# Optimization experiments

Measured on AMD Instinct MI355X. Metric: run time of the kernel, lower is better.

## Reference

```python
import jax, jax.numpy as jnp
import numpy as np

T, B, DIM, LATENT, OUT = 512, 1024, 128, 256, 64


def setup_inputs() -> dict:
    key = jax.random.key(0)
    ks = jax.random.split(key, 6)
    s_i = 1.0 / np.sqrt(DIM)
    s_h = 1.0 / np.sqrt(LATENT)
    return {
        "x": jax.random.normal(ks[0], (T, B, DIM), dtype=jnp.float32),
        "h": jnp.zeros((B, LATENT), dtype=jnp.float32),
        "Wi": jax.random.uniform(ks[1], (DIM, LATENT), jnp.float32, -s_i, s_i),
        "bi": jax.random.uniform(ks[2], (LATENT,), jnp.float32, -s_i, s_i),
        "Wh": jax.random.uniform(ks[3], (LATENT, LATENT), jnp.float32, -s_h, s_h),
        "Wd": jax.random.uniform(ks[4], (LATENT, OUT), jnp.float32, -s_h, s_h),
        "bd": jax.random.uniform(ks[5], (OUT,), jnp.float32, -s_h, s_h),
    }


def reference(x, h, Wi, bi, Wh, Wd, bd):
    # Precompute input projections for all steps in one big GEMM: [T,B,latent]
    xi = jnp.einsum("tbd,dl->tbl", x, Wi) + bi

    def step(h, xi_t):
        h = jnp.tanh(xi_t + h @ Wh)
        return h, None

    h_final, _ = jax.lax.scan(step, h, xi)
    return jax.nn.sigmoid(h_final @ Wd + bd)
```

## Files before the change

### kernel.cpp

```cpp
#include <hip/hip_runtime.h>
#include <cmath>
#include <cstdint>

constexpr int T_STEPS = 512;
constexpr int BATCH   = 1024;
constexpr int DIM     = 128;
constexpr int LATENT  = 256;
constexpr int OUT_DIM = 64;
constexpr int ROWS    = 16;
constexpr int NKSUB   = 48;

typedef __attribute__((ext_vector_type(8))) short bf16x8;
typedef __attribute__((ext_vector_type(4))) float f32x4;

__device__ __forceinline__ uint32_t f2bf(float f) {
    uint32_t u = __builtin_bit_cast(uint32_t, f);
    return (u + 0x7FFFu + ((u >> 16) & 1u)) >> 16;
}
__device__ __forceinline__ float bf2f(uint32_t b) {
    return __builtin_bit_cast(float, b << 16);
}
__device__ __forceinline__ uint32_t pk2(float a, float b) {
    return f2bf(a) | (f2bf(b) << 16);
}
__device__ __forceinline__ float fast_tanh(float v) {
    float e = __builtin_amdgcn_exp2f(v * 2.885390081777927f);
    return __builtin_fmaf(-2.0f, __builtin_amdgcn_rcpf(e + 1.0f), 1.0f);
}
__device__ __forceinline__ float fast_sigmoid(float v) {
    float e = __builtin_amdgcn_exp2f(v * -1.4426950408889634f);
    return __builtin_amdgcn_rcpf(e + 1.0f);
}

__global__ __launch_bounds__(512)
void rnn_mfma_w8t2(const float* __restrict__ x,
                   const float* __restrict__ h0,
                   const float* __restrict__ Wi,
                   const float* __restrict__ bi,
                   const float* __restrict__ Wh,
                   const float* __restrict__ Wd,
                   const float* __restrict__ bd,
                   float* __restrict__ out)
{
    __shared__ uint16_t als[2][NKSUB * 128];

    const int tid   = threadIdx.x;
    const int lane  = tid & 63;
    const int wv    = tid >> 6;
    const int b0    = blockIdx.x * ROWS;
    const int row16 = lane & 15;
    const int kgrp  = lane >> 4;
    const int col0  = (wv << 5) + row16;

#define LOADB(NAME, P)                                                      \
    bf16x8 NAME; {                                                          \
        const float* _p = (P);                                              \
        NAME[0] = (short)f2bf(_p[0]);                                       \
        NAME[1] = (short)f2bf(_p[1 * LATENT]);                              \
        NAME[2] = (short)f2bf(_p[2 * LATENT]);                              \
        NAME[3] = (short)f2bf(_p[3 * LATENT]);                              \
        NAME[4] = (short)f2bf(_p[4 * LATENT]);                              \
        NAME[5] = (short)f2bf(_p[5 * LATENT]);                              \
        NAME[6] = (short)f2bf(_p[6 * LATENT]);                              \
        NAME[7] = (short)f2bf(_p[7 * LATENT]);                              \
    }
#define BPH(KK, CT) (Wh + (size_t)((KK) * 32 + kgrp * 8) * LATENT + col0 + ((CT) << 4))
#define BPX(KK, CT) (Wi + (size_t)(((KK) - 8) * 32 + kgrp * 8) * LATENT + col0 + ((CT) << 4))
#define DECL2H(KK) LOADB(B##KK##_0, BPH(KK,0)) LOADB(B##KK##_1, BPH(KK,1))
#define DECL2X(KK) LOADB(B##KK##_0, BPX(KK,0)) LOADB(B##KK##_1, BPX(KK,1))
    DECL2H(0) DECL2H(1) DECL2H(2)  DECL2H(3)
    DECL2H(4) DECL2H(5) DECL2H(6)  DECL2H(7)
    DECL2X(8) DECL2X(9) DECL2X(10) DECL2X(11)

    const float cb0 = bi[col0];
    const float cb1 = bi[col0 + 16];

    const int pr = tid & 15;
    const int pq = tid >> 4;
    {
        const float* hrow = h0 + (size_t)(b0 + pr) * LATENT + (pq << 3);
        float4 a0 = reinterpret_cast<const float4*>(hrow)[0];
        float4 a1 = reinterpret_cast<const float4*>(hrow)[1];
        *reinterpret_cast<uint4*>(&als[0][(pq * 16 + pr) * 8]) =
            make_uint4(pk2(a0.x, a0.y), pk2(a0.z, a0.w),
                       pk2(a1.x, a1.y), pk2(a1.z, a1.w));
        const float* xrow = x + (size_t)(b0 + pr) * DIM + (pq << 2);
        float4 xv = *reinterpret_cast<const float4*>(xrow);
        uint2* dx = reinterpret_cast<uint2*>(
            &als[0][((32 + (pq >> 1)) * 16 + pr) * 8 + ((pq & 1) << 2)]);
        *dx = make_uint2(pk2(xv.x, xv.y), pk2(xv.z, xv.w));
    }
    __syncthreads();

    const int aoff = kgrp * 128 + row16 * 8;
    const float* xp = x + ((size_t)BATCH + b0 + pr) * DIM + (pq << 2);
    const int xwb = ((32 + (pq >> 1)) * 16 + pr) * 8 + ((pq & 1) << 2);

    int cur = 0;
    for (int t = 0; t < T_STEPS; ++t) {
        const bool pf = (t + 1 < T_STEPS);
        float4 xv;
        if (pf) {
            xv = *reinterpret_cast<const float4*>(xp);
            xp += (size_t)BATCH * DIM;
        }

        f32x4 c0 = {cb0, cb0, cb0, cb0};
        f32x4 c1 = {cb1, cb1, cb1, cb1};
        const uint16_t* ab = &als[cur][aoff];
#define MSTEP(KK) {                                                         \
        const bf16x8 a = *reinterpret_cast<const bf16x8*>(ab + (KK) * 512); \
        c0 = __builtin_amdgcn_mfma_f32_16x16x32_bf16(a, B##KK##_0, c0, 0, 0, 0); \
        c1 = __builtin_amdgcn_mfma_f32_16x16x32_bf16(a, B##KK##_1, c1, 0, 0, 0); }
        MSTEP(0) MSTEP(1) MSTEP(2)  MSTEP(3)
        MSTEP(4) MSTEP(5) MSTEP(6)  MSTEP(7)
        MSTEP(8) MSTEP(9) MSTEP(10) MSTEP(11)

        const int nxt = cur ^ 1;
#define WB(CT, CV) {                                                        \
        const int col = col0 + ((CT) << 4);                                 \
        uint16_t* hw = &als[nxt][(col >> 3) * 128 + (col & 7)];             \
        hw[(kgrp * 4 + 0) * 8] = (uint16_t)f2bf(fast_tanh(CV[0]));          \
        hw[(kgrp * 4 + 1) * 8] = (uint16_t)f2bf(fast_tanh(CV[1]));          \
        hw[(kgrp * 4 + 2) * 8] = (uint16_t)f2bf(fast_tanh(CV[2]));          \
        hw[(kgrp * 4 + 3) * 8] = (uint16_t)f2bf(fast_tanh(CV[3])); }
        WB(0, c0) WB(1, c1)

        if (pf)
            *reinterpret_cast<uint2*>(&als[nxt][xwb]) =
                make_uint2(pk2(xv.x, xv.y), pk2(xv.z, xv.w));

        __syncthreads();
        cur = nxt;
    }

    {
        const int o  = tid & 63;
        const int rb = tid >> 6;
        float s0 = bd[o], s1 = s0;
        const uint16_t* hb = als[cur];
        #pragma unroll 8
        for (int k = 0; k < LATENT; k += 2) {
            const float w0 = Wd[(size_t)k * OUT_DIM + o];
            const float w1 = Wd[(size_t)(k + 1) * OUT_DIM + o];
            const int bx = (k >> 3) * 128 + (k & 7);
            uint32_t p;
            p = *reinterpret_cast<const uint32_t*>(&hb[bx + rb * 8]);
            s0 += bf2f(p & 0xFFFFu) * w0 + bf2f(p >> 16) * w1;
            p = *reinterpret_cast<const uint32_t*>(&hb[bx + (rb + 8) * 8]);
            s1 += bf2f(p & 0xFFFFu) * w0 + bf2f(p >> 16) * w1;
        }
        out[(size_t)(b0 + rb    ) * OUT_DIM + o] = fast_sigmoid(s0);
        out[(size_t)(b0 + rb + 8) * OUT_DIM + o] = fast_sigmoid(s1);
    }
}

extern "C" void kernel_launch(void* const* d_in, const int* in_sizes, int n_in,
                              void* d_out, int out_size, void* d_ws, size_t ws_size,
                              hipStream_t stream) {
    const float* x  = (const float*)d_in[0];
    const float* h0 = (const float*)d_in[1];
    const float* Wi = (const float*)d_in[2];
    const float* bi = (const float*)d_in[3];
    const float* Wh = (const float*)d_in[4];
    const float* Wd = (const float*)d_in[5];
    const float* bd = (const float*)d_in[6];
    float* out = (float*)d_out;

    hipLaunchKernelGGL(rnn_mfma_w8t2, dim3(BATCH / ROWS), dim3(512), 0, stream,
                       x, h0, Wi, bi, Wh, Wd, bd, out);
}
```

Before: 438.7 us.

## Quantize recurrent hidden state and Wh to int8 and use i8 MFMA

Moves the recurrent h@Wh product from bf16 MFMA to int8 MFMA (16x16x64), with Wh quantized per output column and the hidden state stored as int8 with a fixed scale of 127. The input projection stays in bf16, now as a separate accumulator, and LDS is split into swizzled int8 h and bf16 x buffers. This roughly halves the MFMA count and the LDS traffic on the serial recurrence path. The cost is extra accuracy loss from 8-bit hidden states accumulated over 512 steps, plus a dequantize FMA per output.

```diff
diff --git a/kernel.cpp b/kernel.cpp
--- a/kernel.cpp
+++ b/kernel.cpp
@@ -8,18 +8,15 @@
 constexpr int LATENT  = 256;
 constexpr int OUT_DIM = 64;
 constexpr int ROWS    = 16;
-constexpr int NKSUB   = 48;
 
 typedef __attribute__((ext_vector_type(8))) short bf16x8;
 typedef __attribute__((ext_vector_type(4))) float f32x4;
+typedef __attribute__((ext_vector_type(4))) int   i32x4;
 
 __device__ __forceinline__ uint32_t f2bf(float f) {
     uint32_t u = __builtin_bit_cast(uint32_t, f);
     return (u + 0x7FFFu + ((u >> 16) & 1u)) >> 16;
 }
-__device__ __forceinline__ float bf2f(uint32_t b) {
-    return __builtin_bit_cast(float, b << 16);
-}
 __device__ __forceinline__ uint32_t pk2(float a, float b) {
     return f2bf(a) | (f2bf(b) << 16);
 }
@@ -31,70 +28,130 @@
     float e = __builtin_amdgcn_exp2f(v * -1.4426950408889634f);
     return __builtin_amdgcn_rcpf(e + 1.0f);
 }
+__device__ __forceinline__ int q8(float v, float inv) {
+    return (int)__builtin_rintf(v * inv);
+}
+__device__ __forceinline__ uint32_t pack4(int a, int b, int c, int d) {
+    return (uint32_t)(a & 255) | ((uint32_t)(b & 255) << 8) |
+           ((uint32_t)(c & 255) << 16) | ((uint32_t)(d & 255) << 24);
+}
+__device__ __forceinline__ int swz(int sl, int b) {
+    return (sl ^ (b & 3) ^ ((b >> 2) & 3)) & 3;
+}
 
 __global__ __launch_bounds__(512)
-void rnn_mfma_w8t2(const float* __restrict__ x,
-                   const float* __restrict__ h0,
-                   const float* __restrict__ Wi,
-                   const float* __restrict__ bi,
-                   const float* __restrict__ Wh,
-                   const float* __restrict__ Wd,
-                   const float* __restrict__ bd,
-                   float* __restrict__ out)
+void rnn_i8h(const float* __restrict__ x,
+             const float* __restrict__ h0,
+             const float* __restrict__ Wi,
+             const float* __restrict__ bi,
+             const float* __restrict__ Wh,
+             const float* __restrict__ Wd,
+             const float* __restrict__ bd,
+             float* __restrict__ out)
 {
-    __shared__ uint16_t als[2][NKSUB * 128];
-
-    const int tid   = threadIdx.x;
-    const int lane  = tid & 63;
-    const int wv    = tid >> 6;
-    const int b0    = blockIdx.x * ROWS;
-    const int row16 = lane & 15;
-    const int kgrp  = lane >> 4;
-    const int col0  = (wv << 5) + row16;
-
-#define LOADB(NAME, P)                                                      \
+    __shared__ __align__(16) uint8_t hls[2][4096];
+    __shared__ __align__(16) uint8_t xls[2][4096];
+
+    const int tid  = threadIdx.x;
+    const int lane = tid & 63;
+    const int wv   = tid >> 6;
+    const int b0   = blockIdx.x * ROWS;
+    const int b15  = lane & 15;
+    const int kgrp = lane >> 4;
+    const int tg0  = wv * 2, tg1 = wv * 2 + 1;
+    const int wcol0 = tg0 * 16 + b15;
+    const int wcol1 = wcol0 + 16;
+
+    float cmh0 = 0.f, cmh1 = 0.f;
+    {
+        const float* p0 = Wh + (size_t)(kgrp * 16) * LATENT + wcol0;
+        #pragma unroll 4
+        for (int i = 0; i < 64; ++i) {
+            const size_t off = (size_t)((i >> 4) * 64 + (i & 15)) * LATENT;
+            cmh0 = fmaxf(cmh0, fabsf(p0[off]));
+            cmh1 = fmaxf(cmh1, fabsf(p0[off + 16]));
+        }
+        cmh0 = fmaxf(cmh0, __shfl_xor(cmh0, 16));
+        cmh0 = fmaxf(cmh0, __shfl_xor(cmh0, 32));
+        cmh1 = fmaxf(cmh1, __shfl_xor(cmh1, 16));
+        cmh1 = fmaxf(cmh1, __shfl_xor(cmh1, 32));
+    }
+    const float ih0 = cmh0 > 0.f ? 127.f / cmh0 : 0.f;
+    const float ih1 = cmh1 > 0.f ? 127.f / cmh1 : 0.f;
+
+#define WHQ(J) q8(_p[(size_t)(J) * LATENT], _inv)
+#define LOADWH(NAME, WC, S, INV)                                            \
+    i32x4 NAME; {                                                           \
+        const float* _p = Wh + (size_t)((S) * 64 + kgrp * 16) * LATENT + (WC); \
+        const float _inv = (INV);                                           \
+        NAME[0] = (int)pack4(WHQ(0),  WHQ(1),  WHQ(2),  WHQ(3));            \
+        NAME[1] = (int)pack4(WHQ(4),  WHQ(5),  WHQ(6),  WHQ(7));            \
+        NAME[2] = (int)pack4(WHQ(8),  WHQ(9),  WHQ(10), WHQ(11));           \
+        NAME[3] = (int)pack4(WHQ(12), WHQ(13), WHQ(14), WHQ(15));           \
+    }
+    LOADWH(AH0_0, wcol0, 0, ih0) LOADWH(AH0_1, wcol0, 1, ih0)
+    LOADWH(AH0_2, wcol0, 2, ih0) LOADWH(AH0_3, wcol0, 3, ih0)
+    LOADWH(AH1_0, wcol1, 0, ih1) LOADWH(AH1_1, wcol1, 1, ih1)
+    LOADWH(AH1_2, wcol1, 2, ih1) LOADWH(AH1_3, wcol1, 3, ih1)
+
+#define LOADWX(NAME, WC, S)                                                 \
     bf16x8 NAME; {                                                          \
-        const float* _p = (P);                                              \
+        const float* _p = Wi + (size_t)((S) * 32 + kgrp * 8) * LATENT + (WC); \
         NAME[0] = (short)f2bf(_p[0]);                                       \
-        NAME[1] = (short)f2bf(_p[1 * LATENT]);                              \
-        NAME[2] = (short)f2bf(_p[2 * LATENT]);                              \
-        NAME[3] = (short)f2bf(_p[3 * LATENT]);                              \
-        NAME[4] = (short)f2bf(_p[4 * LATENT]);                              \
-        NAME[5] = (short)f2bf(_p[5 * LATENT]);                              \
-        NAME[6] = (short)f2bf(_p[6 * LATENT]);                              \
-        NAME[7] = (short)f2bf(_p[7 * LATENT]);                              \
-    }
-#define BPH(KK, CT) (Wh + (size_t)((KK) * 32 + kgrp * 8) * LATENT + col0 + ((CT) << 4))
-#define BPX(KK, CT) (Wi + (size_t)(((KK) - 8) * 32 + kgrp * 8) * LATENT + col0 + ((CT) << 4))
-#define DECL2H(KK) LOADB(B##KK##_0, BPH(KK,0)) LOADB(B##KK##_1, BPH(KK,1))
-#define DECL2X(KK) LOADB(B##KK##_0, BPX(KK,0)) LOADB(B##KK##_1, BPX(KK,1))
-    DECL2H(0) DECL2H(1) DECL2H(2)  DECL2H(3)
-    DECL2H(4) DECL2H(5) DECL2H(6)  DECL2H(7)
-    DECL2X(8) DECL2X(9) DECL2X(10) DECL2X(11)
-
-    const float cb0 = bi[col0];
-    const float cb1 = bi[col0 + 16];
+        NAME[1] = (short)f2bf(_p[(size_t)1 * LATENT]);                      \
+        NAME[2] = (short)f2bf(_p[(size_t)2 * LATENT]);                      \
+        NAME[3] = (short)f2bf(_p[(size_t)3 * LATENT]);                      \
+        NAME[4] = (short)f2bf(_p[(size_t)4 * LATENT]);                      \
+        NAME[5] = (short)f2bf(_p[(size_t)5 * LATENT]);                      \
+        NAME[6] = (short)f2bf(_p[(size_t)6 * LATENT]);                      \
+        NAME[7] = (short)f2bf(_p[(size_t)7 * LATENT]);                      \
+    }
+    LOADWX(AX0_0, wcol0, 0) LOADWX(AX0_1, wcol0, 1)
+    LOADWX(AX0_2, wcol0, 2) LOADWX(AX0_3, wcol0, 3)
+    LOADWX(AX1_0, wcol1, 0) LOADWX(AX1_1, wcol1, 1)
+    LOADWX(AX1_2, wcol1, 2) LOADWX(AX1_3, wcol1, 3)
+
+    const float dh0_0 = __shfl(cmh0, kgrp * 4 + 0) * (1.f / 16129.f);
+    const float dh0_1 = __shfl(cmh0, kgrp * 4 + 1) * (1.f / 16129.f);
+    const float dh0_2 = __shfl(cmh0, kgrp * 4 + 2) * (1.f / 16129.f);
+    const float dh0_3 = __shfl(cmh0, kgrp * 4 + 3) * (1.f / 16129.f);
+    const float dh1_0 = __shfl(cmh1, kgrp * 4 + 0) * (1.f / 16129.f);
+    const float dh1_1 = __shfl(cmh1, kgrp * 4 + 1) * (1.f / 16129.f);
+    const float dh1_2 = __shfl(cmh1, kgrp * 4 + 2) * (1.f / 16129.f);
+    const float dh1_3 = __shfl(cmh1, kgrp * 4 + 3) * (1.f / 16129.f);
+    const float cb0_0 = bi[tg0 * 16 + kgrp * 4 + 0];
+    const float cb0_1 = bi[tg0 * 16 + kgrp * 4 + 1];
+    const float cb0_2 = bi[tg0 * 16 + kgrp * 4 + 2];
+    const float cb0_3 = bi[tg0 * 16 + kgrp * 4 + 3];
+    const float cb1_0 = bi[tg1 * 16 + kgrp * 4 + 0];
+    const float cb1_1 = bi[tg1 * 16 + kgrp * 4 + 1];
+    const float cb1_2 = bi[tg1 * 16 + kgrp * 4 + 2];
+    const float cb1_3 = bi[tg1 * 16 + kgrp * 4 + 3];
 
     const int pr = tid & 15;
     const int pq = tid >> 4;
+    const int stb = (pq >> 3) * 1024 + pr * 64 +
+                    (swz((pq >> 1) & 3, pr) << 4) + (pq & 1) * 8;
     {
-        const float* hrow = h0 + (size_t)(b0 + pr) * LATENT + (pq << 3);
-        float4 a0 = reinterpret_cast<const float4*>(hrow)[0];
-        float4 a1 = reinterpret_cast<const float4*>(hrow)[1];
-        *reinterpret_cast<uint4*>(&als[0][(pq * 16 + pr) * 8]) =
-            make_uint4(pk2(a0.x, a0.y), pk2(a0.z, a0.w),
-                       pk2(a1.x, a1.y), pk2(a1.z, a1.w));
-        const float* xrow = x + (size_t)(b0 + pr) * DIM + (pq << 2);
-        float4 xv = *reinterpret_cast<const float4*>(xrow);
-        uint2* dx = reinterpret_cast<uint2*>(
-            &als[0][((32 + (pq >> 1)) * 16 + pr) * 8 + ((pq & 1) << 2)]);
-        *dx = make_uint2(pk2(xv.x, xv.y), pk2(xv.z, xv.w));
+        const float* hp = h0 + (size_t)(b0 + pr) * LATENT + pq * 8;
+        uint32_t u0 = pack4(q8(hp[0], 127.f), q8(hp[1], 127.f),
+                            q8(hp[2], 127.f), q8(hp[3], 127.f));
+        uint32_t u1 = pack4(q8(hp[4], 127.f), q8(hp[5], 127.f),
+                            q8(hp[6], 127.f), q8(hp[7], 127.f));
+        *reinterpret_cast<uint2*>(&hls[0][stb]) = make_uint2(u0, u1);
+        const float* xq = x + (size_t)(b0 + pr) * DIM + pq * 4;
+        float4 xv = *reinterpret_cast<const float4*>(xq);
+        *reinterpret_cast<uint2*>(&xls[0][stb]) =
+            make_uint2(pk2(xv.x, xv.y), pk2(xv.z, xv.w));
     }
     __syncthreads();
 
-    const int aoff = kgrp * 128 + row16 * 8;
-    const float* xp = x + ((size_t)BATCH + b0 + pr) * DIM + (pq << 2);
-    const int xwb = ((32 + (pq >> 1)) * 16 + pr) * 8 + ((pq & 1) << 2);
+    const int hrd = b15 * 64 + (swz(kgrp, b15) << 4);
+    const int wb0 = (tg0 >> 2) * 1024 + b15 * 64 +
+                    (swz(tg0 & 3, b15) << 4) + kgrp * 4;
+    const int wb1 = (tg1 >> 2) * 1024 + b15 * 64 +
+                    (swz(tg1 & 3, b15) << 4) + kgrp * 4;
+    const float* xp = x + ((size_t)BATCH + b0 + pr) * DIM + pq * 4;
 
     int cur = 0;
     for (int t = 0; t < T_STEPS; ++t) {
@@ -105,29 +162,57 @@
             xp += (size_t)BATCH * DIM;
         }
 
-        f32x4 c0 = {cb0, cb0, cb0, cb0};
-        f32x4 c1 = {cb1, cb1, cb1, cb1};
-        const uint16_t* ab = &als[cur][aoff];
-#define MSTEP(KK) {                                                         \
-        const bf16x8 a = *reinterpret_cast<const bf16x8*>(ab + (KK) * 512); \
-        c0 = __builtin_amdgcn_mfma_f32_16x16x32_bf16(a, B##KK##_0, c0, 0, 0, 0); \
-        c1 = __builtin_amdgcn_mfma_f32_16x16x32_bf16(a, B##KK##_1, c1, 0, 0, 0); }
-        MSTEP(0) MSTEP(1) MSTEP(2)  MSTEP(3)
-        MSTEP(4) MSTEP(5) MSTEP(6)  MSTEP(7)
-        MSTEP(8) MSTEP(9) MSTEP(10) MSTEP(11)
+        const uint8_t* hb = &hls[cur][hrd];
+        const uint8_t* xb = &xls[cur][hrd];
+        i32x4  bh0 = *reinterpret_cast<const i32x4*>(hb);
+        i32x4  bh1 = *reinterpret_cast<const i32x4*>(hb + 1024);
+        i32x4  bh2 = *reinterpret_cast<const i32x4*>(hb + 2048);
+        i32x4  bh3 = *reinterpret_cast<const i32x4*>(hb + 3072);
+        bf16x8 bx0 = *reinterpret_cast<const bf16x8*>(xb);
+        bf16x8 bx1 = *reinterpret_cast<const bf16x8*>(xb + 1024);
+        bf16x8 bx2 = *reinterpret_cast<const bf16x8*>(xb + 2048);
+        bf16x8 bx3 = *reinterpret_cast<const bf16x8*>(xb + 3072);
+
+        i32x4 ch0 = {0, 0, 0, 0}, ch1 = {0, 0, 0, 0};
+        f32x4 cx0 = {cb0_0, cb0_1, cb0_2, cb0_3};
+        f32x4 cx1 = {cb1_0, cb1_1, cb1_2, cb1_3};
+
+        ch0 = __builtin_amdgcn_mfma_i32_16x16x64_i8(AH0_0, bh0, ch0, 0, 0, 0);
+        ch1 = __builtin_amdgcn_mfma_i32_16x16x64_i8(AH1_0, bh0, ch1, 0, 0, 0);
+        cx0 = __builtin_amdgcn_mfma_f32_16x16x32_bf16(AX0_0, bx0, cx0, 0, 0, 0);
+        cx1 = __builtin_amdgcn_mfma_f32_16x16x32_bf16(AX1_0, bx0, cx1, 0, 0, 0);
+        ch0 = __builtin_amdgcn_mfma_i32_16x16x64_i8(AH0_1, bh1, ch0, 0, 0, 0);
+        ch1 = __builtin_amdgcn_mfma_i32_16x16x64_i8(AH1_1, bh1, ch1, 0, 0, 0);
+        cx0 = __builtin_amdgcn_mfma_f32_16x16x32_bf16(AX0_1, bx1, cx0, 0, 0, 0);
+        cx1 = __builtin_amdgcn_mfma_f32_16x16x32_bf16(AX1_1, bx1, cx1, 0, 0, 0);
+        ch0 = __builtin_amdgcn_mfma_i32_16x16x64_i8(AH0_2, bh2, ch0, 0, 0, 0);
+        ch1 = __builtin_amdgcn_mfma_i32_16x16x64_i8(AH1_2, bh2, ch1, 0, 0, 0);
+        cx0 = __builtin_amdgcn_mfma_f32_16x16x32_bf16(AX0_2, bx2, cx0, 0, 0, 0);
+        cx1 = __builtin_amdgcn_mfma_f32_16x16x32_bf16(AX1_2, bx2, cx1, 0, 0, 0);
+        ch0 = __builtin_amdgcn_mfma_i32_16x16x64_i8(AH0_3, bh3, ch0, 0, 0, 0);
+        ch1 = __builtin_amdgcn_mfma_i32_16x16x64_i8(AH1_3, bh3, ch1, 0, 0, 0);
+        cx0 = __builtin_amdgcn_mfma_f32_16x16x32_bf16(AX0_3, bx3, cx0, 0, 0, 0);
+        cx1 = __builtin_amdgcn_mfma_f32_16x16x32_bf16(AX1_3, bx3, cx1, 0, 0, 0);
 
         const int nxt = cur ^ 1;
-#define WB(CT, CV) {                                                        \
-        const int col = col0 + ((CT) << 4);                                 \
-        uint16_t* hw = &als[nxt][(col >> 3) * 128 + (col & 7)];             \
-        hw[(kgrp * 4 + 0) * 8] = (uint16_t)f2bf(fast_tanh(CV[0]));          \
-        hw[(kgrp * 4 + 1) * 8] = (uint16_t)f2bf(fast_tanh(CV[1]));          \
-        hw[(kgrp * 4 + 2) * 8] = (uint16_t)f2bf(fast_tanh(CV[2]));          \
-        hw[(kgrp * 4 + 3) * 8] = (uint16_t)f2bf(fast_tanh(CV[3])); }
-        WB(0, c0) WB(1, c1)
-
+        {
+            float v0 = fast_tanh(__builtin_fmaf((float)ch0[0], dh0_0, cx0[0]));
+            float v1 = fast_tanh(__builtin_fmaf((float)ch0[1], dh0_1, cx0[1]));
+            float v2 = fast_tanh(__builtin_fmaf((float)ch0[2], dh0_2, cx0[2]));
+            float v3 = fast_tanh(__builtin_fmaf((float)ch0[3], dh0_3, cx0[3]));
+            *reinterpret_cast<uint32_t*>(&hls[nxt][wb0]) =
+                pack4(q8(v0, 127.f), q8(v1, 127.f), q8(v2, 127.f), q8(v3, 127.f));
+        }
+        {
+            float v0 = fast_tanh(__builtin_fmaf((float)ch1[0], dh1_0, cx1[0]));
+            float v1 = fast_tanh(__builtin_fmaf((float)ch1[1], dh1_1, cx1[1]));
+            float v2 = fast_tanh(__builtin_fmaf((float)ch1[2], dh1_2, cx1[2]));
+            float v3 = fast_tanh(__builtin_fmaf((float)ch1[3], dh1_3, cx1[3]));
+            *reinterpret_cast<uint32_t*>(&hls[nxt][wb1]) =
+                pack4(q8(v0, 127.f), q8(v1, 127.f), q8(v2, 127.f), q8(v3, 127.f));
+        }
         if (pf)
-            *reinterpret_cast<uint2*>(&als[nxt][xwb]) =
+            *reinterpret_cast<uint2*>(&xls[nxt][stb]) =
                 make_uint2(pk2(xv.x, xv.y), pk2(xv.z, xv.w));
 
         __syncthreads();
@@ -137,21 +222,28 @@
     {
         const int o  = tid & 63;
         const int rb = tid >> 6;
-        float s0 = bd[o], s1 = s0;
-        const uint16_t* hb = als[cur];
-        #pragma unroll 8
-        for (int k = 0; k < LATENT; k += 2) {
-            const float w0 = Wd[(size_t)k * OUT_DIM + o];
+        float s0 = 0.f, s1 = 0.f;
+        #pragma unroll 4
+        for (int k = 0; k < LATENT; k += 4) {
+            const int sl   = (k >> 4) & 3;
+            const int base = (k >> 6) * 1024 + (k & 15);
+            const uint32_t pA = *reinterpret_cast<const uint32_t*>(
+                &hls[cur][base + rb * 64 + (swz(sl, rb) << 4)]);
+            const uint32_t pB = *reinterpret_cast<const uint32_t*>(
+                &hls[cur][base + (rb + 8) * 64 + (swz(sl, rb + 8) << 4)]);
+            const float w0 = Wd[(size_t)(k + 0) * OUT_DIM + o];
             const float w1 = Wd[(size_t)(k + 1) * OUT_DIM + o];
-            const int bx = (k >> 3) * 128 + (k & 7);
-            uint32_t p;
-            p = *reinterpret_cast<const uint32_t*>(&hb[bx + rb * 8]);
-            s0 += bf2f(p & 0xFFFFu) * w0 + bf2f(p >> 16) * w1;
-            p = *reinterpret_cast<const uint32_t*>(&hb[bx + (rb + 8) * 8]);
-            s1 += bf2f(p & 0xFFFFu) * w0 + bf2f(p >> 16) * w1;
-        }
-        out[(size_t)(b0 + rb    ) * OUT_DIM + o] = fast_sigmoid(s0);
-        out[(size_t)(b0 + rb + 8) * OUT_DIM + o] = fast_sigmoid(s1);
+            const float w2 = Wd[(size_t)(k + 2) * OUT_DIM + o];
+            const float w3 = Wd[(size_t)(k + 3) * OUT_DIM + o];
+            s0 += (float)(int8_t)(pA) * w0 + (float)(int8_t)(pA >> 8) * w1
+                + (float)(int8_t)(pA >> 16) * w2 + (float)(int8_t)(pA >> 24) * w3;
+            s1 += (float)(int8_t)(pB) * w0 + (float)(int8_t)(pB >> 8) * w1
+                + (float)(int8_t)(pB >> 16) * w2 + (float)(int8_t)(pB >> 24) * w3;
+        }
+        out[(size_t)(b0 + rb) * OUT_DIM + o] =
+            fast_sigmoid(bd[o] + s0 * (1.f / 127.f));
+        out[(size_t)(b0 + rb + 8) * OUT_DIM + o] =
+            fast_sigmoid(bd[o] + s1 * (1.f / 127.f));
     }
 }
 
@@ -167,6 +259,6 @@
     const float* bd = (const float*)d_in[6];
     float* out = (float*)d_out;
 
-    hipLaunchKernelGGL(rnn_mfma_w8t2, dim3(BATCH / ROWS), dim3(512), 0, stream,
+    hipLaunchKernelGGL(rnn_i8h, dim3(BATCH / ROWS), dim3(512), 0, stream,
                        x, h0, Wi, bi, Wh, Wd, bd, out);
 }
```

New measurement: 402.8 us (median of 3 runs). 8.2% less time.
